# Performance work log

Measured on AMD Instinct MI355X. Metric: run time of the kernel, lower is better.

Reference implementation:

```python
import jax, jax.numpy as jnp
import numpy as np

N_QUBITS = 8

def _ry(theta):
    # PennyLane RY = exp(-i theta Y/2) = [[c,-s],[s,c]]
    c = jnp.cos(theta / 2).astype(jnp.complex64)
    s = jnp.sin(theta / 2).astype(jnp.complex64)
    return jnp.stack([jnp.stack([c, -s], -1), jnp.stack([s, c], -1)], -2)

def _rz(theta):
    # PennyLane RZ = diag(e^{-i theta/2}, e^{i theta/2})
    ph = jnp.exp(-0.5j * theta.astype(jnp.complex64))
    z = jnp.zeros_like(ph)
    return jnp.stack([jnp.stack([ph, z], -1), jnp.stack([z, jnp.conj(ph)], -1)], -2)

def _apply_1q(state, U, wire):
    # state: (B, 2,...,2); U: (2,2) or (B,2,2)
    state = jnp.moveaxis(state, wire + 1, -1)
    if U.ndim == 3:
        state = jnp.einsum('bij,b...j->b...i', U, state)
    else:
        state = jnp.einsum('ij,b...j->b...i', U, state)
    return jnp.moveaxis(state, -1, wire + 1)

def _apply_cnot(state, c, t):
    state = jnp.moveaxis(state, (c + 1, t + 1), (-2, -1))
    state = jnp.concatenate([state[..., 0:1, :], state[..., 1:2, ::-1]], axis=-2)
    return jnp.moveaxis(state, (-2, -1), (c + 1, t + 1))

def _circuit(angles, qw):
    # angles: (B, 2*n_qubits), qw: (3, n_qubits, 3)
    B = angles.shape[0]
    state = jnp.zeros((B,) + (2,) * N_QUBITS, jnp.complex64)
    state = state.at[(slice(None),) + (0,) * N_QUBITS].set(1.0)
    for i in range(N_QUBITS):
        state = _apply_1q(state, _ry(angles[:, i]), i)
        state = _apply_1q(state, _rz(angles[:, i + N_QUBITS]), i)
    for layer in range(3):
        for i in range(N_QUBITS):
            phi, theta, omega = qw[layer, i]
            U = _rz(omega) @ _ry(theta) @ _rz(phi)  # Rot(phi,theta,omega)
            state = _apply_1q(state, U, i)
        for i in range(N_QUBITS - 1):
            state = _apply_cnot(state, i, i + 1)
        state = _apply_cnot(state, N_QUBITS - 1, 0)
    probs = jnp.abs(state) ** 2  # (B, 2,...,2) real
    expz = []
    for i in range(N_QUBITS):
        p = probs.sum(axis=tuple(a for a in range(1, N_QUBITS + 1) if a != i + 1))
        expz.append(p[:, 0] - p[:, 1])  # <Z_i> = p(0) - p(1)
    return jnp.stack(expz, -1)


def setup_inputs() -> dict:
    key = jax.random.key(0)
    ks = jax.random.split(key, 10)
    B = 16384
    return {
        'x': jax.random.normal(ks[0], (B, 80), jnp.float32),
        'W1': jax.random.normal(ks[1], (64, 80), jnp.float32) * 0.1,
        'b1': jax.random.normal(ks[2], (64,), jnp.float32) * 0.1,
        'W2': jax.random.normal(ks[3], (32, 64), jnp.float32) * 0.1,
        'b2': jax.random.normal(ks[4], (32,), jnp.float32) * 0.1,
        'W3': jax.random.normal(ks[5], (16, 32), jnp.float32) * 0.1,
        'b3': jax.random.normal(ks[6], (16,), jnp.float32) * 0.1,
        'qw': jax.random.normal(ks[7], (3, 8, 3), jnp.float32),
        'Wp': jax.random.normal(ks[8], (128, 8), jnp.float32) * 0.1,
        'bp': jax.random.normal(ks[9], (128,), jnp.float32) * 0.1,
    }


def reference(x, W1, b1, W2, b2, W3, b3, qw, Wp, bp):
    h = jnp.tanh(x @ W1.T + b1)
    h = jnp.tanh(h @ W2.T + b2)
    angles = h @ W3.T + b3          # (B, 16)
    z = _circuit(angles, qw)        # (B, 8) PauliZ expectations
    return z @ Wp.T + bp            # (B, 128)
```

## Files before the change

kernel.cpp:

```cpp
#include <hip/hip_runtime.h>

typedef float v2f __attribute__((ext_vector_type(2)));

#define WPB 4
#define NE  4

__device__ __forceinline__ float xorf(float v, int sb) {
  return __int_as_float(__float_as_int(v) ^ sb);
}
__device__ __forceinline__ v2f xor2(v2f v, int sb) {
  return (v2f){xorf(v.x, sb), xorf(v.y, sb)};
}

__device__ __forceinline__ void pkfma_ip(v2f a, v2f b, v2f& acc) {
  asm("v_pk_fma_f32 %0, %1, %2, %0" : "+v"(acc) : "v"(a), "v"(b));
}
__device__ __forceinline__ v2f pkmul_bl(v2f c, v2f v) {
  v2f r; asm("v_pk_mul_f32 %0, %1, %2 op_sel:[0,0] op_sel_hi:[0,1]"
             : "=v"(r) : "v"(c), "v"(v)); return r;
}
__device__ __forceinline__ void pkfma_bl(v2f c, v2f v, v2f& acc) {
  asm("v_pk_fma_f32 %0, %1, %2, %0 op_sel:[0,0,0] op_sel_hi:[0,1,1]"
      : "+v"(acc) : "v"(c), "v"(v));
}
__device__ __forceinline__ void pkfma_bl_n(v2f c, v2f v, v2f& acc) {
  asm("v_pk_fma_f32 %0, %1, %2, %0 op_sel:[0,0,0] op_sel_hi:[0,1,1] neg_lo:[1,0,0] neg_hi:[1,0,0]"
      : "+v"(acc) : "v"(c), "v"(v));
}
__device__ __forceinline__ void pkfma_bh_i(v2f c, v2f v, v2f& acc) {
  asm("v_pk_fma_f32 %0, %1, %2, %0 op_sel:[1,1,0] op_sel_hi:[1,0,1] neg_lo:[1,0,0]"
      : "+v"(acc) : "v"(c), "v"(v));
}
__device__ __forceinline__ void pkfma_bh_mi(v2f c, v2f v, v2f& acc) {
  asm("v_pk_fma_f32 %0, %1, %2, %0 op_sel:[1,1,0] op_sel_hi:[1,0,1] neg_hi:[1,0,0]"
      : "+v"(acc) : "v"(c), "v"(v));
}
__device__ __forceinline__ v2f cmul(v2f a, v2f b) {
  v2f r = pkmul_bl(a, b);
  pkfma_bh_i(a, b, r);
  return r;
}

template<int M>
__device__ __forceinline__ float xch(float v, int a32) {
  if constexpr (M == 32)
    return __int_as_float(__builtin_amdgcn_ds_bpermute(a32, __float_as_int(v)));
  else if constexpr (M == 16 || M == 4)
    return __int_as_float(__builtin_amdgcn_ds_swizzle(__float_as_int(v), (M << 10) | 0x1f));
  else if constexpr (M == 8) {
    int i = __float_as_int(v);
    return __int_as_float(__builtin_amdgcn_update_dpp(i, i, 0x128, 0xF, 0xF, false));
  } else if constexpr (M == 2) {
    int i = __float_as_int(v);
    return __int_as_float(__builtin_amdgcn_update_dpp(i, i, 0x4E, 0xF, 0xF, false));
  } else {
    int i = __float_as_int(v);
    return __int_as_float(__builtin_amdgcn_update_dpp(i, i, 0xB1, 0xF, 0xF, false));
  }
}
template<int M>
__device__ __forceinline__ v2f xch2(v2f v, int a32) {
  v2f r; r.x = xch<M>(v.x, a32); r.y = xch<M>(v.y, a32); return r;
}
__device__ __forceinline__ v2f bperm2(int addr, v2f v) {
  v2f r;
  r.x = __int_as_float(__builtin_amdgcn_ds_bpermute(addr, __float_as_int(v.x)));
  r.y = __int_as_float(__builtin_amdgcn_ds_bpermute(addr, __float_as_int(v.y)));
  return r;
}

__device__ __forceinline__ void gpair(v2f& a, v2f& b, v2f P1, v2f P2) {
  v2f na = pkmul_bl(P1, a);
  pkfma_bh_i(P1, a, na);
  pkfma_bl(P2, b, na);
  pkfma_bh_i(P2, b, na);
  v2f nb = pkmul_bl(P1, b);
  pkfma_bh_mi(P1, b, nb);
  pkfma_bl_n(P2, a, nb);
  pkfma_bh_i(P2, a, nb);
  a = na; b = nb;
}
__device__ __forceinline__ v2f glane(v2f a, v2f p, v2f P1, v2f P2) {
  v2f t = pkmul_bl(P1, a);
  pkfma_bh_i(P1, a, t);
  pkfma_bl(P2, p, t);
  pkfma_bh_i(P2, p, t);
  return t;
}

template<int W>
__device__ __forceinline__ void gate_elem(v2f& S0, v2f& S1, v2f& S2, v2f& S3,
                                          v2f P1, v2f P2, int a32) {
  if constexpr (W == 0)      { gpair(S0, S2, P1, P2); gpair(S1, S3, P1, P2); }
  else if constexpr (W == 1) { gpair(S0, S1, P1, P2); gpair(S2, S3, P1, P2); }
  else {
    constexpr int M = 1 << (7 - W);
    v2f p0 = xch2<M>(S0, a32), p1 = xch2<M>(S1, a32),
        p2 = xch2<M>(S2, a32), p3 = xch2<M>(S3, a32);
    S0 = glane(S0, p0, P1, P2); S1 = glane(S1, p1, P1, P2);
    S2 = glane(S2, p2, P1, P2); S3 = glane(S3, p3, P1, P2);
  }
}

__device__ __forceinline__ void build_state(v2f& S0, v2f& S1, v2f& S2, v2f& S3,
                                            const float4* csW, int lane) {
  v2f g2, g3, g4, g5, g6, g7;
  #define BG(q, dst) { float4 c = csW[q]; \
    v2f P1 = (v2f){c.x, c.y}; v2f nc2 = (v2f){-c.z, c.w}; \
    dst = (((lane >> (7 - (q))) & 1) != 0) ? nc2 : P1; }
  BG(2, g2) BG(3, g3) BG(4, g4) BG(5, g5) BG(6, g6) BG(7, g7)
  #undef BG
  v2f common = cmul(cmul(cmul(g2, g3), cmul(g4, g5)), cmul(g6, g7));
  float4 c0 = csW[0], c1 = csW[1];
  v2f P10 = (v2f){c0.x, c0.y}, m0 = (v2f){-c0.z, c0.w};
  v2f P11 = (v2f){c1.x, c1.y}, m1 = (v2f){-c1.z, c1.w};
  S0 = cmul(cmul(P10, P11), common);
  S1 = cmul(cmul(P10, m1 ), common);
  S2 = cmul(cmul(m0 , P11), common);
  S3 = cmul(cmul(m0 , m1 ), common);
}

__device__ __forceinline__ void cnot_ring(v2f& S0, v2f& S1, v2f& S2, v2f& S3,
                                          int addrA, int addrB, int lane) {
  { v2f t = S2; S2 = S3; S3 = t; }
  S0 = bperm2(addrA, S0); S2 = bperm2(addrA, S2);
  S1 = bperm2(addrB, S1); S3 = bperm2(addrB, S3);
  bool c0 = (lane & 1) != 0;
  v2f t0 = S0, t1 = S1;
  S0 = c0 ? S2 : S0; S2 = c0 ? t0 : S2;
  S1 = c0 ? S3 : S1; S3 = c0 ? t1 : S3;
}

__device__ __forceinline__ void readout2(v2f A0, v2f A1, v2f A2, v2f A3,
                                         v2f B0, v2f B1, v2f B2, v2f B3,
                                         int lane, const int* sb, int a32,
                                         v2f& z0, v2f& z1, v2f& z2, v2f& z3,
                                         v2f& z4, v2f& z5, v2f& z6, v2f& z7) {
  v2f p0 = (v2f){fmaf(A0.x,A0.x,A0.y*A0.y), fmaf(B0.x,B0.x,B0.y*B0.y)};
  v2f p1 = (v2f){fmaf(A1.x,A1.x,A1.y*A1.y), fmaf(B1.x,B1.x,B1.y*B1.y)};
  v2f p2 = (v2f){fmaf(A2.x,A2.x,A2.y*A2.y), fmaf(B2.x,B2.x,B2.y*B2.y)};
  v2f p3 = (v2f){fmaf(A3.x,A3.x,A3.y*A3.y), fmaf(B3.x,B3.x,B3.y*B3.y)};
  v2f E = (p0 + p3) - (p1 + p2);
  v2f F = (p0 + p2) - (p1 + p3);
  v2f Fv = xor2(F, (__popc(lane) & 1) << 31);
  v2f Sm = E, d1, d2, d3, d4, d5, d6;
  { v2f p = xch2<32>(Sm, a32); d1 = xor2(Sm - p, sb[0]); Sm += p; }
  { v2f p = xch2<16>(Sm, a32); Sm += p;
    v2f q = xch2<16>(d1, a32); d2 = xor2(d1 - q, sb[1]); d1 += q; }
  { v2f p = xch2<8>(Sm, a32); Sm += p;
    v2f q = xch2<8>(d1, a32); d1 += q;
    v2f r = xch2<8>(d2, a32); d3 = xor2(d2 - r, sb[2]); d2 += r; }
  { v2f p = xch2<4>(Sm, a32); Sm += p;
    v2f q = xch2<4>(d1, a32); d1 += q;
    v2f r = xch2<4>(d2, a32); d2 += r;
    v2f t = xch2<4>(d3, a32); d4 = xor2(d3 - t, sb[3]); d3 += t; }
  { v2f p = xch2<2>(Sm, a32); Sm += p;
    v2f q = xch2<2>(d1, a32); d1 += q;
    v2f r = xch2<2>(d2, a32); d2 += r;
    v2f t = xch2<2>(d3, a32); d3 += t;
    v2f w = xch2<2>(d4, a32); d5 = xor2(d4 - w, sb[4]); d4 += w; }
  { v2f p = xch2<1>(Sm, a32); Sm += p;
    v2f q = xch2<1>(d1, a32); d1 += q;
    v2f r = xch2<1>(d2, a32); d2 += r;
    v2f t = xch2<1>(d3, a32); d3 += t;
    v2f w = xch2<1>(d4, a32); d4 += w;
    v2f v = xch2<1>(d5, a32); d6 = xor2(d5 - v, sb[5]); d5 += v; }
  Fv += xch2<32>(Fv, a32); Fv += xch2<16>(Fv, a32); Fv += xch2<8>(Fv, a32);
  Fv += xch2<4>(Fv, a32);  Fv += xch2<2>(Fv, a32);  Fv += xch2<1>(Fv, a32);
  z0 = Fv; z1 = Sm; z2 = d1; z3 = d2;
  z4 = d3; z5 = d4; z6 = d5; z7 = d6;
}

__device__ __forceinline__ float fast_tanh(float x) {
  float e = __expf(2.f * x);
  return 1.f - 2.f * __builtin_amdgcn_rcpf(e + 1.f);
}
__device__ __forceinline__ v2f vlo(float4 v) { return (v2f){v.x, v.y}; }
__device__ __forceinline__ v2f vhi(float4 v) { return (v2f){v.z, v.w}; }

__global__ void prep_rot_kernel(const float* __restrict__ qw, float* __restrict__ U) {
  int t = threadIdx.x;
  if (t < 24) {
    float phi = qw[t*3+0], theta = qw[t*3+1], omega = qw[t*3+2];
    float st, ct; sincosf(0.5f*theta, &st, &ct);
    float sa, ca; sincosf(0.5f*(phi+omega), &sa, &ca);
    float sd, cd; sincosf(0.5f*(phi-omega), &sd, &cd);
    float4 o; o.x = ct*ca; o.y = -ct*sa; o.z = -st*cd; o.w = -st*sd;
    ((float4*)U)[t] = o;
  }
}

__global__ __launch_bounds__(64*WPB, 4) void qblock_kernel(
    const float* __restrict__ x,  const float* __restrict__ W1, const float* __restrict__ b1,
    const float* __restrict__ W2, const float* __restrict__ b2,
    const float* __restrict__ W3, const float* __restrict__ b3,
    const float* __restrict__ Urot, const float* __restrict__ Wp, const float* __restrict__ bp,
    float* __restrict__ out, int B4)
{
  __shared__ float  h1s[WPB][NE][64];
  __shared__ float  h2s[WPB][NE][32];
  __shared__ v2f    cs [WPB][NE][16];
  __shared__ float4 csW[WPB][NE][8];

  const int lane = threadIdx.x & 63;
  const int wv   = threadIdx.x >> 6;
  int bw = blockIdx.x * WPB + wv;
  if (bw >= B4) bw = B4 - 1;
  bw = __builtin_amdgcn_readfirstlane(bw);
  const int e0 = NE * bw;
  const v2f* Ug2 = (const v2f*)Urot;

  {
    const float4* wr = (const float4*)(W1 + lane * 80);
    float bv = b1[lane];
    v2f a0A = (v2f){bv,0.f}, a1A = (v2f){0.f,0.f};
    v2f a0B = a0A, a1B = a1A, a0C = a0A, a1C = a1A, a0D = a0A, a1D = a1A;
    #pragma unroll
    for (int k = 0; k < 20; ++k) {
      float4 wk = wr[k];
      #define L1E(E, e) { \
        float4 xk = ((const float4*)(x + (size_t)(e0 + (e)) * 80))[k]; \
        pkfma_ip(vlo(xk), vlo(wk), a0##E); pkfma_ip(vhi(xk), vhi(wk), a1##E); }
      L1E(A,0) L1E(B,1) L1E(C,2) L1E(D,3)
      #undef L1E
    }
    h1s[wv][0][lane] = fast_tanh((a0A.x + a0A.y) + (a1A.x + a1A.y));
    h1s[wv][1][lane] = fast_tanh((a0B.x + a0B.y) + (a1B.x + a1B.y));
    h1s[wv][2][lane] = fast_tanh((a0C.x + a0C.y) + (a1C.x + a1C.y));
    h1s[wv][3][lane] = fast_tanh((a0D.x + a0D.y) + (a1D.x + a1D.y));
  }
  __threadfence_block();

  {
    const int ep = lane >> 5, row = lane & 31;
    const float4* wr = (const float4*)(W2 + row * 64);
    const float4* hvA = (const float4*)(&h1s[wv][2*ep+0][0]);
    const float4* hvB = (const float4*)(&h1s[wv][2*ep+1][0]);
    v2f aA0 = (v2f){b2[row], 0.f}, aA1 = (v2f){0.f, 0.f};
    v2f aB0 = aA0, aB1 = aA1;
    #pragma unroll
    for (int k = 0; k < 16; ++k) {
      float4 wk = wr[k], hA = hvA[k], hB = hvB[k];
      pkfma_ip(vlo(hA), vlo(wk), aA0); pkfma_ip(vhi(hA), vhi(wk), aA1);
      pkfma_ip(vlo(hB), vlo(wk), aB0); pkfma_ip(vhi(hB), vhi(wk), aB1);
    }
    h2s[wv][2*ep+0][row] = fast_tanh((aA0.x + aA0.y) + (aA1.x + aA1.y));
    h2s[wv][2*ep+1][row] = fast_tanh((aB0.x + aB0.y) + (aB1.x + aB1.y));
  }
  __threadfence_block();

  {
    const int e = lane >> 4, row = lane & 15;
    const float4* hv = (const float4*)(&h2s[wv][e][0]);
    const float4* wr = (const float4*)(W3 + row * 32);
    v2f ac0 = (v2f){b3[row], 0.f}, ac1 = (v2f){0.f, 0.f};
    #pragma unroll
    for (int k = 0; k < 8; ++k) {
      float4 hk = hv[k], wk = wr[k];
      pkfma_ip(vlo(hk), vlo(wk), ac0);
      pkfma_ip(vhi(hk), vhi(wk), ac1);
    }
    float sh, ch; __sincosf(0.5f * ((ac0.x + ac0.y) + (ac1.x + ac1.y)), &sh, &ch);
    cs[wv][e][row] = (v2f){ch, sh};
  }
  __threadfence_block();

  if (lane < 32) {
    const int e = lane >> 3, k = lane & 7;
    v2f yy = cs[wv][e][k], zz = cs[wv][e][k + 8];
    v2f u1 = (v2f){  yy.x * zz.x, -yy.x * zz.y };
    v2f u2 = (v2f){ -yy.y * zz.x,  yy.y * zz.y };
    v2f cu1 = (v2f){ u1.x, -u1.y };
    v2f cu2 = (v2f){ u2.x, -u2.y };
    v2f r1 = Ug2[2 * k], r2 = Ug2[2 * k + 1];
    v2f P1c = cmul(r1, u1);
    pkfma_bl_n(r2, cu2, P1c);
    pkfma_bh_mi(r2, cu2, P1c);
    v2f P2c = cmul(r1, u2);
    pkfma_bl(r2, cu1, P2c);
    pkfma_bh_i(r2, cu1, P2c);
    csW[wv][e][k] = make_float4(P1c.x, P1c.y, P2c.x, P2c.y);
  }
  __threadfence_block();

  const int a32 = (lane ^ 32) << 2;
  const int sb[6] = { (lane&32)<<26, (lane&16)<<27, (lane&8)<<28,
                      (lane&4)<<29, (lane&2)<<30, (lane&1)<<31 };
  const int addrA = ((lane ^ (lane >> 1)) & 63) << 2;
  const int addrB = addrA ^ 128;

  v2f sA0, sA1, sA2, sA3, sB0, sB1, sB2, sB3;
  v2f sC0, sC1, sC2, sC3, sD0, sD1, sD2, sD3;
  build_state(sA0, sA1, sA2, sA3, &csW[wv][0][0], lane);
  build_state(sB0, sB1, sB2, sB3, &csW[wv][1][0], lane);
  build_state(sC0, sC1, sC2, sC3, &csW[wv][2][0], lane);
  build_state(sD0, sD1, sD2, sD3, &csW[wv][3][0], lane);
  #define RING_ALL \
    cnot_ring(sA0, sA1, sA2, sA3, addrA, addrB, lane); \
    cnot_ring(sB0, sB1, sB2, sB3, addrA, addrB, lane); \
    cnot_ring(sC0, sC1, sC2, sC3, addrA, addrB, lane); \
    cnot_ring(sD0, sD1, sD2, sD3, addrA, addrB, lane);
  RING_ALL

  #define LG(l, i) { \
    v2f P1 = Ug2[((l)*8+(i))*2], P2 = Ug2[((l)*8+(i))*2+1]; \
    if constexpr ((i) >= 2) { \
      P1.y = xorf(P1.y, sb[(i)-2]); P2.x = xorf(P2.x, sb[(i)-2]); } \
    gate_elem<i>(sA0, sA1, sA2, sA3, P1, P2, a32); \
    gate_elem<i>(sB0, sB1, sB2, sB3, P1, P2, a32); \
    gate_elem<i>(sC0, sC1, sC2, sC3, P1, P2, a32); \
    gate_elem<i>(sD0, sD1, sD2, sD3, P1, P2, a32); }
  LG(1,0) LG(1,1) LG(1,2) LG(1,3) LG(1,4) LG(1,5) LG(1,6) LG(1,7)
  RING_ALL
  LG(2,0) LG(2,1) LG(2,2) LG(2,3) LG(2,4) LG(2,5) LG(2,6) LG(2,7)
  #undef LG
  #undef RING_ALL

  const int r0 = 2 * lane;
  const float4* wp = (const float4*)(Wp + r0 * 8);
  float4 w0v = wp[0], w1v = wp[1], w2v = wp[2], w3v = wp[3];
  float2 bpv = ((const float2*)bp)[lane];
  #define PROJ_STORE(eA, eB) { \
    v2f o0 = (v2f){bpv.x, bpv.x}; \
    v2f o1 = (v2f){bpv.y, bpv.y}; \
    o0 += z0*w0v.x + z1*w0v.y + z2*w0v.z + z3*w0v.w \
        + z4*w1v.x + z5*w1v.y + z6*w1v.z + z7*w1v.w; \
    o1 += z0*w2v.x + z1*w2v.y + z2*w2v.z + z3*w2v.w \
        + z4*w3v.x + z5*w3v.y + z6*w3v.z + z7*w3v.w; \
    ((float2*)(out + (size_t)(e0 + (eA)) * 128))[lane] = make_float2(o0.x, o1.x); \
    ((float2*)(out + (size_t)(e0 + (eB)) * 128))[lane] = make_float2(o0.y, o1.y); }
  {
    v2f z0, z1, z2, z3, z4, z5, z6, z7;
    readout2(sA0, sA1, sA2, sA3, sB0, sB1, sB2, sB3, lane, sb, a32,
             z0, z1, z2, z3, z4, z5, z6, z7);
    PROJ_STORE(0, 1)
  }
  {
    v2f z0, z1, z2, z3, z4, z5, z6, z7;
    readout2(sC0, sC1, sC2, sC3, sD0, sD1, sD2, sD3, lane, sb, a32,
             z0, z1, z2, z3, z4, z5, z6, z7);
    PROJ_STORE(2, 3)
  }
  #undef PROJ_STORE
}

extern "C" void kernel_launch(void* const* d_in, const int* in_sizes, int n_in,
                              void* d_out, int out_size, void* d_ws, size_t ws_size,
                              hipStream_t stream) {
  const float* x  = (const float*)d_in[0];
  const float* W1 = (const float*)d_in[1];
  const float* b1 = (const float*)d_in[2];
  const float* W2 = (const float*)d_in[3];
  const float* b2 = (const float*)d_in[4];
  const float* W3 = (const float*)d_in[5];
  const float* b3 = (const float*)d_in[6];
  const float* qw = (const float*)d_in[7];
  const float* Wp = (const float*)d_in[8];
  const float* bp = (const float*)d_in[9];
  float* out = (float*)d_out;
  float* Urot = (float*)d_ws;

  const int B = in_sizes[0] / 80;
  const int B4 = B / NE;
  prep_rot_kernel<<<1, 64, 0, stream>>>(qw, Urot);
  const int grid = (B4 + WPB - 1) / WPB;
  qblock_kernel<<<grid, 64 * WPB, 0, stream>>>(x, W1, b1, W2, b2, W3, b3,
                                               Urot, Wp, bp, out, B4);
}
```

Before: 41.79 us.

## Split fused kernel into MLP prep kernel and per-element circuit kernel

Splits the single fused kernel in two. The first kernel computes the MLP and the initial rotation coefficients and writes them to a global workspace. The second runs the quantum circuit with one element per wavefront instead of four, which reduces register pressure and gives four times as many waves for latency hiding. The cost is an extra launch, a global round trip for the coefficients, and the loss of the four-element interleaving that gave instruction-level parallelism and packed readout.

```diff
diff --git a/kernel.cpp b/kernel.cpp
--- a/kernel.cpp
+++ b/kernel.cpp
@@ -7,9 +7,6 @@
 
 __device__ __forceinline__ float xorf(float v, int sb) {
   return __int_as_float(__float_as_int(v) ^ sb);
-}
-__device__ __forceinline__ v2f xor2(v2f v, int sb) {
-  return (v2f){xorf(v.x, sb), xorf(v.y, sb)};
 }
 
 __device__ __forceinline__ void pkfma_ip(v2f a, v2f b, v2f& acc) {
@@ -131,46 +128,6 @@
   S1 = c0 ? S3 : S1; S3 = c0 ? t1 : S3;
 }
 
-__device__ __forceinline__ void readout2(v2f A0, v2f A1, v2f A2, v2f A3,
-                                         v2f B0, v2f B1, v2f B2, v2f B3,
-                                         int lane, const int* sb, int a32,
-                                         v2f& z0, v2f& z1, v2f& z2, v2f& z3,
-                                         v2f& z4, v2f& z5, v2f& z6, v2f& z7) {
-  v2f p0 = (v2f){fmaf(A0.x,A0.x,A0.y*A0.y), fmaf(B0.x,B0.x,B0.y*B0.y)};
-  v2f p1 = (v2f){fmaf(A1.x,A1.x,A1.y*A1.y), fmaf(B1.x,B1.x,B1.y*B1.y)};
-  v2f p2 = (v2f){fmaf(A2.x,A2.x,A2.y*A2.y), fmaf(B2.x,B2.x,B2.y*B2.y)};
-  v2f p3 = (v2f){fmaf(A3.x,A3.x,A3.y*A3.y), fmaf(B3.x,B3.x,B3.y*B3.y)};
-  v2f E = (p0 + p3) - (p1 + p2);
-  v2f F = (p0 + p2) - (p1 + p3);
-  v2f Fv = xor2(F, (__popc(lane) & 1) << 31);
-  v2f Sm = E, d1, d2, d3, d4, d5, d6;
-  { v2f p = xch2<32>(Sm, a32); d1 = xor2(Sm - p, sb[0]); Sm += p; }
-  { v2f p = xch2<16>(Sm, a32); Sm += p;
-    v2f q = xch2<16>(d1, a32); d2 = xor2(d1 - q, sb[1]); d1 += q; }
-  { v2f p = xch2<8>(Sm, a32); Sm += p;
-    v2f q = xch2<8>(d1, a32); d1 += q;
-    v2f r = xch2<8>(d2, a32); d3 = xor2(d2 - r, sb[2]); d2 += r; }
-  { v2f p = xch2<4>(Sm, a32); Sm += p;
-    v2f q = xch2<4>(d1, a32); d1 += q;
-    v2f r = xch2<4>(d2, a32); d2 += r;
-    v2f t = xch2<4>(d3, a32); d4 = xor2(d3 - t, sb[3]); d3 += t; }
-  { v2f p = xch2<2>(Sm, a32); Sm += p;
-    v2f q = xch2<2>(d1, a32); d1 += q;
-    v2f r = xch2<2>(d2, a32); d2 += r;
-    v2f t = xch2<2>(d3, a32); d3 += t;
-    v2f w = xch2<2>(d4, a32); d5 = xor2(d4 - w, sb[4]); d4 += w; }
-  { v2f p = xch2<1>(Sm, a32); Sm += p;
-    v2f q = xch2<1>(d1, a32); d1 += q;
-    v2f r = xch2<1>(d2, a32); d2 += r;
-    v2f t = xch2<1>(d3, a32); d3 += t;
-    v2f w = xch2<1>(d4, a32); d4 += w;
-    v2f v = xch2<1>(d5, a32); d6 = xor2(d5 - v, sb[5]); d5 += v; }
-  Fv += xch2<32>(Fv, a32); Fv += xch2<16>(Fv, a32); Fv += xch2<8>(Fv, a32);
-  Fv += xch2<4>(Fv, a32);  Fv += xch2<2>(Fv, a32);  Fv += xch2<1>(Fv, a32);
-  z0 = Fv; z1 = Sm; z2 = d1; z3 = d2;
-  z4 = d3; z5 = d4; z6 = d5; z7 = d6;
-}
-
 __device__ __forceinline__ float fast_tanh(float x) {
   float e = __expf(2.f * x);
   return 1.f - 2.f * __builtin_amdgcn_rcpf(e + 1.f);
@@ -190,17 +147,15 @@
   }
 }
 
-__global__ __launch_bounds__(64*WPB, 4) void qblock_kernel(
+__global__ __launch_bounds__(64*WPB) void prep_kernel(
     const float* __restrict__ x,  const float* __restrict__ W1, const float* __restrict__ b1,
     const float* __restrict__ W2, const float* __restrict__ b2,
     const float* __restrict__ W3, const float* __restrict__ b3,
-    const float* __restrict__ Urot, const float* __restrict__ Wp, const float* __restrict__ bp,
-    float* __restrict__ out, int B4)
+    const float* __restrict__ Urot, float4* __restrict__ csWg, int B4)
 {
-  __shared__ float  h1s[WPB][NE][64];
-  __shared__ float  h2s[WPB][NE][32];
-  __shared__ v2f    cs [WPB][NE][16];
-  __shared__ float4 csW[WPB][NE][8];
+  __shared__ float h1s[WPB][NE][64];
+  __shared__ float h2s[WPB][NE][32];
+  __shared__ v2f   cs [WPB][NE][16];
 
   const int lane = threadIdx.x & 63;
   const int wv   = threadIdx.x >> 6;
@@ -279,9 +234,21 @@
     v2f P2c = cmul(r1, u2);
     pkfma_bl(r2, cu1, P2c);
     pkfma_bh_i(r2, cu1, P2c);
-    csW[wv][e][k] = make_float4(P1c.x, P1c.y, P2c.x, P2c.y);
-  }
-  __threadfence_block();
+    csWg[(size_t)(e0 + e) * 8 + k] = make_float4(P1c.x, P1c.y, P2c.x, P2c.y);
+  }
+}
+
+__global__ __launch_bounds__(64*WPB) void qcirc_kernel(
+    const float* __restrict__ Urot, const float4* __restrict__ csWg,
+    const float* __restrict__ Wp, const float* __restrict__ bp,
+    float* __restrict__ out, int B)
+{
+  const int lane = threadIdx.x & 63;
+  const int wv   = threadIdx.x >> 6;
+  int e = blockIdx.x * WPB + wv;
+  if (e >= B) e = B - 1;
+  e = __builtin_amdgcn_readfirstlane(e);
+  const v2f* Ug2 = (const v2f*)Urot;
 
   const int a32 = (lane ^ 32) << 2;
   const int sb[6] = { (lane&32)<<26, (lane&16)<<27, (lane&8)<<28,
@@ -289,59 +256,62 @@
   const int addrA = ((lane ^ (lane >> 1)) & 63) << 2;
   const int addrB = addrA ^ 128;
 
-  v2f sA0, sA1, sA2, sA3, sB0, sB1, sB2, sB3;
-  v2f sC0, sC1, sC2, sC3, sD0, sD1, sD2, sD3;
-  build_state(sA0, sA1, sA2, sA3, &csW[wv][0][0], lane);
-  build_state(sB0, sB1, sB2, sB3, &csW[wv][1][0], lane);
-  build_state(sC0, sC1, sC2, sC3, &csW[wv][2][0], lane);
-  build_state(sD0, sD1, sD2, sD3, &csW[wv][3][0], lane);
-  #define RING_ALL \
-    cnot_ring(sA0, sA1, sA2, sA3, addrA, addrB, lane); \
-    cnot_ring(sB0, sB1, sB2, sB3, addrA, addrB, lane); \
-    cnot_ring(sC0, sC1, sC2, sC3, addrA, addrB, lane); \
-    cnot_ring(sD0, sD1, sD2, sD3, addrA, addrB, lane);
-  RING_ALL
+  v2f s0, s1, s2, s3;
+  build_state(s0, s1, s2, s3, csWg + (size_t)e * 8, lane);
+  cnot_ring(s0, s1, s2, s3, addrA, addrB, lane);
 
   #define LG(l, i) { \
     v2f P1 = Ug2[((l)*8+(i))*2], P2 = Ug2[((l)*8+(i))*2+1]; \
     if constexpr ((i) >= 2) { \
       P1.y = xorf(P1.y, sb[(i)-2]); P2.x = xorf(P2.x, sb[(i)-2]); } \
-    gate_elem<i>(sA0, sA1, sA2, sA3, P1, P2, a32); \
-    gate_elem<i>(sB0, sB1, sB2, sB3, P1, P2, a32); \
-    gate_elem<i>(sC0, sC1, sC2, sC3, P1, P2, a32); \
-    gate_elem<i>(sD0, sD1, sD2, sD3, P1, P2, a32); }
+    gate_elem<i>(s0, s1, s2, s3, P1, P2, a32); }
   LG(1,0) LG(1,1) LG(1,2) LG(1,3) LG(1,4) LG(1,5) LG(1,6) LG(1,7)
-  RING_ALL
+  cnot_ring(s0, s1, s2, s3, addrA, addrB, lane);
   LG(2,0) LG(2,1) LG(2,2) LG(2,3) LG(2,4) LG(2,5) LG(2,6) LG(2,7)
   #undef LG
-  #undef RING_ALL
+
+  float p0 = s0.x*s0.x + s0.y*s0.y;
+  float p1 = s1.x*s1.x + s1.y*s1.y;
+  float p2 = s2.x*s2.x + s2.y*s2.y;
+  float p3 = s3.x*s3.x + s3.y*s3.y;
+  float E = (p0 + p3) - (p1 + p2);
+  float F = (p0 + p2) - (p1 + p3);
+  float Fv = xorf(F, (__popc(lane) & 1) << 31);
+  float Sm = E, d1, d2, d3, d4, d5, d6;
+  { float p = xch<32>(Sm, a32); d1 = xorf(Sm - p, sb[0]); Sm += p; }
+  { float p = xch<16>(Sm, a32); Sm += p;
+    float q = xch<16>(d1, a32); d2 = xorf(d1 - q, sb[1]); d1 += q; }
+  { float p = xch<8>(Sm, a32); Sm += p;
+    float q = xch<8>(d1, a32); d1 += q;
+    float r = xch<8>(d2, a32); d3 = xorf(d2 - r, sb[2]); d2 += r; }
+  { float p = xch<4>(Sm, a32); Sm += p;
+    float q = xch<4>(d1, a32); d1 += q;
+    float r = xch<4>(d2, a32); d2 += r;
+    float t = xch<4>(d3, a32); d4 = xorf(d3 - t, sb[3]); d3 += t; }
+  { float p = xch<2>(Sm, a32); Sm += p;
+    float q = xch<2>(d1, a32); d1 += q;
+    float r = xch<2>(d2, a32); d2 += r;
+    float t = xch<2>(d3, a32); d3 += t;
+    float w = xch<2>(d4, a32); d5 = xorf(d4 - w, sb[4]); d4 += w; }
+  { float p = xch<1>(Sm, a32); Sm += p;
+    float q = xch<1>(d1, a32); d1 += q;
+    float r = xch<1>(d2, a32); d2 += r;
+    float t = xch<1>(d3, a32); d3 += t;
+    float w = xch<1>(d4, a32); d4 += w;
+    float v = xch<1>(d5, a32); d6 = xorf(d5 - v, sb[5]); d5 += v; }
+  Fv += xch<32>(Fv, a32); Fv += xch<16>(Fv, a32); Fv += xch<8>(Fv, a32);
+  Fv += xch<4>(Fv, a32);  Fv += xch<2>(Fv, a32);  Fv += xch<1>(Fv, a32);
+  const float z0 = Fv, z1 = Sm, z2 = d1, z3 = d2, z4 = d3, z5 = d4, z6 = d5, z7 = d6;
 
   const int r0 = 2 * lane;
   const float4* wp = (const float4*)(Wp + r0 * 8);
   float4 w0v = wp[0], w1v = wp[1], w2v = wp[2], w3v = wp[3];
   float2 bpv = ((const float2*)bp)[lane];
-  #define PROJ_STORE(eA, eB) { \
-    v2f o0 = (v2f){bpv.x, bpv.x}; \
-    v2f o1 = (v2f){bpv.y, bpv.y}; \
-    o0 += z0*w0v.x + z1*w0v.y + z2*w0v.z + z3*w0v.w \
-        + z4*w1v.x + z5*w1v.y + z6*w1v.z + z7*w1v.w; \
-    o1 += z0*w2v.x + z1*w2v.y + z2*w2v.z + z3*w2v.w \
-        + z4*w3v.x + z5*w3v.y + z6*w3v.z + z7*w3v.w; \
-    ((float2*)(out + (size_t)(e0 + (eA)) * 128))[lane] = make_float2(o0.x, o1.x); \
-    ((float2*)(out + (size_t)(e0 + (eB)) * 128))[lane] = make_float2(o0.y, o1.y); }
-  {
-    v2f z0, z1, z2, z3, z4, z5, z6, z7;
-    readout2(sA0, sA1, sA2, sA3, sB0, sB1, sB2, sB3, lane, sb, a32,
-             z0, z1, z2, z3, z4, z5, z6, z7);
-    PROJ_STORE(0, 1)
-  }
-  {
-    v2f z0, z1, z2, z3, z4, z5, z6, z7;
-    readout2(sC0, sC1, sC2, sC3, sD0, sD1, sD2, sD3, lane, sb, a32,
-             z0, z1, z2, z3, z4, z5, z6, z7);
-    PROJ_STORE(2, 3)
-  }
-  #undef PROJ_STORE
+  float o0 = bpv.x + z0*w0v.x + z1*w0v.y + z2*w0v.z + z3*w0v.w
+                   + z4*w1v.x + z5*w1v.y + z6*w1v.z + z7*w1v.w;
+  float o1 = bpv.y + z0*w2v.x + z1*w2v.y + z2*w2v.z + z3*w2v.w
+                   + z4*w3v.x + z5*w3v.y + z6*w3v.z + z7*w3v.w;
+  ((float2*)(out + (size_t)e * 128))[lane] = make_float2(o0, o1);
 }
 
 extern "C" void kernel_launch(void* const* d_in, const int* in_sizes, int n_in,
@@ -359,11 +329,13 @@
   const float* bp = (const float*)d_in[9];
   float* out = (float*)d_out;
   float* Urot = (float*)d_ws;
+  float4* csWg = (float4*)((char*)d_ws + 1024);
 
   const int B = in_sizes[0] / 80;
   const int B4 = B / NE;
   prep_rot_kernel<<<1, 64, 0, stream>>>(qw, Urot);
-  const int grid = (B4 + WPB - 1) / WPB;
-  qblock_kernel<<<grid, 64 * WPB, 0, stream>>>(x, W1, b1, W2, b2, W3, b3,
-                                               Urot, Wp, bp, out, B4);
-}
+  prep_kernel<<<(B4 + WPB - 1) / WPB, 64 * WPB, 0, stream>>>(
+      x, W1, b1, W2, b2, W3, b3, Urot, csWg, B4);
+  qcirc_kernel<<<(B + WPB - 1) / WPB, 64 * WPB, 0, stream>>>(
+      Urot, csWg, Wp, bp, out, B);
+}
```

After: 46.87 us. +12.2%, slower.

## Replace per-sample gate simulation with bf16 MFMA complex matmul against precomputed circuit unitary

Applied to the files above, without the earlier changes.

The fixed trainable part of the circuit (two variational layers plus CNOT rings) is now precomputed once per call as a 256x256 complex unitary in bf16 by a separate kernel. Each block builds the encoded product states of 16 samples in LDS and multiplies them by the unitary using bf16 MFMA, then reduces signed probabilities into Z expectations. W1/W2 are also transposed into LDS for coalesced MLP loads. This trades the shuffle-heavy per-gate work for matrix-core throughput, at the cost of bf16 precision loss, an extra kernel launch and heavy global/LDS traffic streaming the 256 KB unitary through every block.

```diff
diff --git a/kernel.cpp b/kernel.cpp
--- a/kernel.cpp
+++ b/kernel.cpp
@@ -1,15 +1,16 @@
 #include <hip/hip_runtime.h>
 
 typedef float v2f __attribute__((ext_vector_type(2)));
+typedef float f32x4 __attribute__((ext_vector_type(4)));
+typedef short bf16x8 __attribute__((ext_vector_type(8)));
 
 #define WPB 4
 #define NE  4
 
+#define SE(E,N) s##E##N
+
 __device__ __forceinline__ float xorf(float v, int sb) {
   return __int_as_float(__float_as_int(v) ^ sb);
-}
-__device__ __forceinline__ v2f xor2(v2f v, int sb) {
-  return (v2f){xorf(v.x, sb), xorf(v.y, sb)};
 }
 
 __device__ __forceinline__ void pkfma_ip(v2f a, v2f b, v2f& acc) {
@@ -87,7 +88,6 @@
   pkfma_bh_i(P2, p, t);
   return t;
 }
-
 template<int W>
 __device__ __forceinline__ void gate_elem(v2f& S0, v2f& S1, v2f& S2, v2f& S3,
                                           v2f P1, v2f P2, int a32) {
@@ -101,7 +101,15 @@
     S2 = glane(S2, p2, P1, P2); S3 = glane(S3, p3, P1, P2);
   }
 }
-
+__device__ __forceinline__ void cnot_ring(v2f& S0, v2f& S1, v2f& S2, v2f& S3,
+                                          int addrA, int addrB, int lane) {
+  { v2f t = S2; S2 = S3; S3 = t; }
+  v2f q0 = bperm2(addrA, S0), q2 = bperm2(addrA, S2);
+  v2f q1 = bperm2(addrB, S1), q3 = bperm2(addrB, S3);
+  bool c0 = (lane & 1) != 0;
+  S0 = c0 ? q2 : q0; S2 = c0 ? q0 : q2;
+  S1 = c0 ? q3 : q1; S3 = c0 ? q1 : q3;
+}
 __device__ __forceinline__ void build_state(v2f& S0, v2f& S1, v2f& S2, v2f& S3,
                                             const float4* csW, int lane) {
   v2f g2, g3, g4, g5, g6, g7;
@@ -120,63 +128,17 @@
   S3 = cmul(cmul(m0 , m1 ), common);
 }
 
-__device__ __forceinline__ void cnot_ring(v2f& S0, v2f& S1, v2f& S2, v2f& S3,
-                                          int addrA, int addrB, int lane) {
-  { v2f t = S2; S2 = S3; S3 = t; }
-  S0 = bperm2(addrA, S0); S2 = bperm2(addrA, S2);
-  S1 = bperm2(addrB, S1); S3 = bperm2(addrB, S3);
-  bool c0 = (lane & 1) != 0;
-  v2f t0 = S0, t1 = S1;
-  S0 = c0 ? S2 : S0; S2 = c0 ? t0 : S2;
-  S1 = c0 ? S3 : S1; S3 = c0 ? t1 : S3;
-}
-
-__device__ __forceinline__ void readout2(v2f A0, v2f A1, v2f A2, v2f A3,
-                                         v2f B0, v2f B1, v2f B2, v2f B3,
-                                         int lane, const int* sb, int a32,
-                                         v2f& z0, v2f& z1, v2f& z2, v2f& z3,
-                                         v2f& z4, v2f& z5, v2f& z6, v2f& z7) {
-  v2f p0 = (v2f){fmaf(A0.x,A0.x,A0.y*A0.y), fmaf(B0.x,B0.x,B0.y*B0.y)};
-  v2f p1 = (v2f){fmaf(A1.x,A1.x,A1.y*A1.y), fmaf(B1.x,B1.x,B1.y*B1.y)};
-  v2f p2 = (v2f){fmaf(A2.x,A2.x,A2.y*A2.y), fmaf(B2.x,B2.x,B2.y*B2.y)};
-  v2f p3 = (v2f){fmaf(A3.x,A3.x,A3.y*A3.y), fmaf(B3.x,B3.x,B3.y*B3.y)};
-  v2f E = (p0 + p3) - (p1 + p2);
-  v2f F = (p0 + p2) - (p1 + p3);
-  v2f Fv = xor2(F, (__popc(lane) & 1) << 31);
-  v2f Sm = E, d1, d2, d3, d4, d5, d6;
-  { v2f p = xch2<32>(Sm, a32); d1 = xor2(Sm - p, sb[0]); Sm += p; }
-  { v2f p = xch2<16>(Sm, a32); Sm += p;
-    v2f q = xch2<16>(d1, a32); d2 = xor2(d1 - q, sb[1]); d1 += q; }
-  { v2f p = xch2<8>(Sm, a32); Sm += p;
-    v2f q = xch2<8>(d1, a32); d1 += q;
-    v2f r = xch2<8>(d2, a32); d3 = xor2(d2 - r, sb[2]); d2 += r; }
-  { v2f p = xch2<4>(Sm, a32); Sm += p;
-    v2f q = xch2<4>(d1, a32); d1 += q;
-    v2f r = xch2<4>(d2, a32); d2 += r;
-    v2f t = xch2<4>(d3, a32); d4 = xor2(d3 - t, sb[3]); d3 += t; }
-  { v2f p = xch2<2>(Sm, a32); Sm += p;
-    v2f q = xch2<2>(d1, a32); d1 += q;
-    v2f r = xch2<2>(d2, a32); d2 += r;
-    v2f t = xch2<2>(d3, a32); d3 += t;
-    v2f w = xch2<2>(d4, a32); d5 = xor2(d4 - w, sb[4]); d4 += w; }
-  { v2f p = xch2<1>(Sm, a32); Sm += p;
-    v2f q = xch2<1>(d1, a32); d1 += q;
-    v2f r = xch2<1>(d2, a32); d2 += r;
-    v2f t = xch2<1>(d3, a32); d3 += t;
-    v2f w = xch2<1>(d4, a32); d4 += w;
-    v2f v = xch2<1>(d5, a32); d6 = xor2(d5 - v, sb[5]); d5 += v; }
-  Fv += xch2<32>(Fv, a32); Fv += xch2<16>(Fv, a32); Fv += xch2<8>(Fv, a32);
-  Fv += xch2<4>(Fv, a32);  Fv += xch2<2>(Fv, a32);  Fv += xch2<1>(Fv, a32);
-  z0 = Fv; z1 = Sm; z2 = d1; z3 = d2;
-  z4 = d3; z5 = d4; z6 = d5; z7 = d6;
-}
-
 __device__ __forceinline__ float fast_tanh(float x) {
   float e = __expf(2.f * x);
   return 1.f - 2.f * __builtin_amdgcn_rcpf(e + 1.f);
 }
 __device__ __forceinline__ v2f vlo(float4 v) { return (v2f){v.x, v.y}; }
 __device__ __forceinline__ v2f vhi(float4 v) { return (v2f){v.z, v.w}; }
+__device__ __forceinline__ unsigned short bf16rne(float f) {
+  unsigned int u = __float_as_uint(f);
+  u += 0x7fffu + ((u >> 16) & 1u);
+  return (unsigned short)(u >> 16);
+}
 
 __global__ void prep_rot_kernel(const float* __restrict__ qw, float* __restrict__ U) {
   int t = threadIdx.x;
@@ -190,68 +152,161 @@
   }
 }
 
-__global__ __launch_bounds__(64*WPB, 4) void qblock_kernel(
+__global__ __launch_bounds__(256) void prep_U_kernel(
+    const float* __restrict__ Urot,
+    unsigned short* __restrict__ UTre, unsigned short* __restrict__ UTim)
+{
+  const int lane = threadIdx.x & 63;
+  const int wv   = threadIdx.x >> 6;
+  const int base = blockIdx.x * 16 + wv * 4;
+  const v2f* Ug2 = (const v2f*)Urot;
+
+  const int a32 = (lane ^ 32) << 2;
+  const int sb[6] = { (lane&32)<<26, (lane&16)<<27, (lane&8)<<28,
+                      (lane&4)<<29, (lane&2)<<30, (lane&1)<<31 };
+  const int addrA = ((lane ^ (lane >> 1)) & 63) << 2;
+  const int addrB = addrA ^ 128;
+
+  v2f sA0,sA1,sA2,sA3, sB0,sB1,sB2,sB3, sC0,sC1,sC2,sC3, sD0,sD1,sD2,sD3;
+  #define INITB(E, q) { int b = base + (q); \
+    float one = (lane == (b & 63)) ? 1.f : 0.f; \
+    SE(E,0) = (v2f){((b>>6)==0)?one:0.f, 0.f}; \
+    SE(E,1) = (v2f){((b>>6)==1)?one:0.f, 0.f}; \
+    SE(E,2) = (v2f){((b>>6)==2)?one:0.f, 0.f}; \
+    SE(E,3) = (v2f){((b>>6)==3)?one:0.f, 0.f}; }
+  INITB(A,0) INITB(B,1) INITB(C,2) INITB(D,3)
+  #undef INITB
+
+  #define RING_ALL \
+    cnot_ring(sA0, sA1, sA2, sA3, addrA, addrB, lane); \
+    cnot_ring(sB0, sB1, sB2, sB3, addrA, addrB, lane); \
+    cnot_ring(sC0, sC1, sC2, sC3, addrA, addrB, lane); \
+    cnot_ring(sD0, sD1, sD2, sD3, addrA, addrB, lane);
+  #define LG(l, i) { \
+    v2f P1 = Ug2[((l)*8+(i))*2], P2 = Ug2[((l)*8+(i))*2+1]; \
+    if constexpr ((i) >= 2) { \
+      P1.y = xorf(P1.y, sb[(i)-2]); P2.x = xorf(P2.x, sb[(i)-2]); } \
+    gate_elem<i>(sA0, sA1, sA2, sA3, P1, P2, a32); \
+    gate_elem<i>(sB0, sB1, sB2, sB3, P1, P2, a32); \
+    gate_elem<i>(sC0, sC1, sC2, sC3, P1, P2, a32); \
+    gate_elem<i>(sD0, sD1, sD2, sD3, P1, P2, a32); }
+  RING_ALL
+  LG(1,0) LG(1,1) LG(1,2) LG(1,3) LG(1,4) LG(1,5) LG(1,6) LG(1,7)
+  RING_ALL
+  LG(2,0) LG(2,1) LG(2,2) LG(2,3) LG(2,4) LG(2,5) LG(2,6) LG(2,7)
+  #undef LG
+  #undef RING_ALL
+
+  #define STOREB(E, q) { int b = base + (q); \
+    UTre[(0*64+lane)*256 + b] = bf16rne(SE(E,0).x); UTim[(0*64+lane)*256 + b] = bf16rne(SE(E,0).y); \
+    UTre[(1*64+lane)*256 + b] = bf16rne(SE(E,1).x); UTim[(1*64+lane)*256 + b] = bf16rne(SE(E,1).y); \
+    UTre[(2*64+lane)*256 + b] = bf16rne(SE(E,2).x); UTim[(2*64+lane)*256 + b] = bf16rne(SE(E,2).y); \
+    UTre[(3*64+lane)*256 + b] = bf16rne(SE(E,3).x); UTim[(3*64+lane)*256 + b] = bf16rne(SE(E,3).y); }
+  STOREB(A,0) STOREB(B,1) STOREB(C,2) STOREB(D,3)
+  #undef STOREB
+}
+
+#define OFF_ARE 0
+#define OFF_AIM 8192
+#define OFF_BRE 16384
+#define OFF_BIM 32768
+#define OFF_W1T 0
+#define OFF_W2T 20480
+#define OFF_H1  28672
+#define OFF_H2  32768
+#define OFF_CS  34816
+#define OFF_CSW 36864
+#define OFF_ZL  0
+
+__global__ __launch_bounds__(256) void qblock_kernel(
     const float* __restrict__ x,  const float* __restrict__ W1, const float* __restrict__ b1,
     const float* __restrict__ W2, const float* __restrict__ b2,
     const float* __restrict__ W3, const float* __restrict__ b3,
-    const float* __restrict__ Urot, const float* __restrict__ Wp, const float* __restrict__ bp,
-    float* __restrict__ out, int B4)
+    const float* __restrict__ Urot,
+    const unsigned short* __restrict__ UTre, const unsigned short* __restrict__ UTim,
+    const float* __restrict__ Wp, const float* __restrict__ bp,
+    float* __restrict__ out)
 {
-  __shared__ float  h1s[WPB][NE][64];
-  __shared__ float  h2s[WPB][NE][32];
-  __shared__ v2f    cs [WPB][NE][16];
-  __shared__ float4 csW[WPB][NE][8];
-
-  const int lane = threadIdx.x & 63;
-  const int wv   = threadIdx.x >> 6;
-  int bw = blockIdx.x * WPB + wv;
-  if (bw >= B4) bw = B4 - 1;
-  bw = __builtin_amdgcn_readfirstlane(bw);
-  const int e0 = NE * bw;
+  __shared__ char smem[49152];
+  v2f*            W1t = (v2f*)(smem + OFF_W1T);
+  v2f*            W2t = (v2f*)(smem + OFF_W2T);
+  float*          h1s = (float*)(smem + OFF_H1);
+  float*          h2s = (float*)(smem + OFF_H2);
+  v2f*            csv = (v2f*)(smem + OFF_CS);
+  float4*         csW = (float4*)(smem + OFF_CSW);
+  unsigned short* Are = (unsigned short*)(smem + OFF_ARE);
+  unsigned short* Aim = (unsigned short*)(smem + OFF_AIM);
+  unsigned short* Bre = (unsigned short*)(smem + OFF_BRE);
+  unsigned short* Bim = (unsigned short*)(smem + OFF_BIM);
+  float*          zl  = (float*)(smem + OFF_ZL);
+
+  const int tid  = threadIdx.x;
+  const int lane = tid & 63;
+  const int wv   = tid >> 6;
+  const int e0   = blockIdx.x * 16;
+  const int ew   = e0 + wv * NE;
   const v2f* Ug2 = (const v2f*)Urot;
 
   {
-    const float4* wr = (const float4*)(W1 + lane * 80);
+    const v2f* W1f2 = (const v2f*)W1;
+    #pragma unroll
+    for (int i = 0; i < 10; ++i) {
+      int j = i * 256 + tid;
+      int r = j / 40, kk = j - r * 40;
+      W1t[kk * 64 + r] = W1f2[j];
+    }
+    const v2f* W2f2 = (const v2f*)W2;
+    #pragma unroll
+    for (int i = 0; i < 4; ++i) {
+      int j = i * 256 + tid;
+      int r = j >> 5, kk = j & 31;
+      W2t[kk * 32 + r] = W2f2[j];
+    }
+  }
+  __syncthreads();
+
+  {
+    const v2f* xA = (const v2f*)(x + (size_t)(ew + 0) * 80);
+    const v2f* xB = (const v2f*)(x + (size_t)(ew + 1) * 80);
+    const v2f* xC = (const v2f*)(x + (size_t)(ew + 2) * 80);
+    const v2f* xD = (const v2f*)(x + (size_t)(ew + 3) * 80);
     float bv = b1[lane];
-    v2f a0A = (v2f){bv,0.f}, a1A = (v2f){0.f,0.f};
-    v2f a0B = a0A, a1B = a1A, a0C = a0A, a1C = a1A, a0D = a0A, a1D = a1A;
-    #pragma unroll
-    for (int k = 0; k < 20; ++k) {
-      float4 wk = wr[k];
-      #define L1E(E, e) { \
-        float4 xk = ((const float4*)(x + (size_t)(e0 + (e)) * 80))[k]; \
-        pkfma_ip(vlo(xk), vlo(wk), a0##E); pkfma_ip(vhi(xk), vhi(wk), a1##E); }
-      L1E(A,0) L1E(B,1) L1E(C,2) L1E(D,3)
-      #undef L1E
-    }
-    h1s[wv][0][lane] = fast_tanh((a0A.x + a0A.y) + (a1A.x + a1A.y));
-    h1s[wv][1][lane] = fast_tanh((a0B.x + a0B.y) + (a1B.x + a1B.y));
-    h1s[wv][2][lane] = fast_tanh((a0C.x + a0C.y) + (a1C.x + a1C.y));
-    h1s[wv][3][lane] = fast_tanh((a0D.x + a0D.y) + (a1D.x + a1D.y));
+    v2f aA = (v2f){bv, 0.f}, aB = aA, aC = aA, aD = aA;
+    #pragma unroll 8
+    for (int kk = 0; kk < 40; ++kk) {
+      v2f w = W1t[kk * 64 + lane];
+      pkfma_ip(w, xA[kk], aA);
+      pkfma_ip(w, xB[kk], aB);
+      pkfma_ip(w, xC[kk], aC);
+      pkfma_ip(w, xD[kk], aD);
+    }
+    h1s[(wv*4+0)*64 + lane] = fast_tanh(aA.x + aA.y);
+    h1s[(wv*4+1)*64 + lane] = fast_tanh(aB.x + aB.y);
+    h1s[(wv*4+2)*64 + lane] = fast_tanh(aC.x + aC.y);
+    h1s[(wv*4+3)*64 + lane] = fast_tanh(aD.x + aD.y);
   }
   __threadfence_block();
 
   {
     const int ep = lane >> 5, row = lane & 31;
-    const float4* wr = (const float4*)(W2 + row * 64);
-    const float4* hvA = (const float4*)(&h1s[wv][2*ep+0][0]);
-    const float4* hvB = (const float4*)(&h1s[wv][2*ep+1][0]);
-    v2f aA0 = (v2f){b2[row], 0.f}, aA1 = (v2f){0.f, 0.f};
-    v2f aB0 = aA0, aB1 = aA1;
-    #pragma unroll
-    for (int k = 0; k < 16; ++k) {
-      float4 wk = wr[k], hA = hvA[k], hB = hvB[k];
-      pkfma_ip(vlo(hA), vlo(wk), aA0); pkfma_ip(vhi(hA), vhi(wk), aA1);
-      pkfma_ip(vlo(hB), vlo(wk), aB0); pkfma_ip(vhi(hB), vhi(wk), aB1);
-    }
-    h2s[wv][2*ep+0][row] = fast_tanh((aA0.x + aA0.y) + (aA1.x + aA1.y));
-    h2s[wv][2*ep+1][row] = fast_tanh((aB0.x + aB0.y) + (aB1.x + aB1.y));
+    const v2f* hA = (const v2f*)(&h1s[(wv*4 + 2*ep+0)*64]);
+    const v2f* hB = (const v2f*)(&h1s[(wv*4 + 2*ep+1)*64]);
+    float bv = b2[row];
+    v2f aA = (v2f){bv, 0.f}, aB = aA;
+    #pragma unroll 8
+    for (int kk = 0; kk < 32; ++kk) {
+      v2f w = W2t[kk * 32 + row];
+      pkfma_ip(w, hA[kk], aA);
+      pkfma_ip(w, hB[kk], aB);
+    }
+    h2s[(wv*4 + 2*ep+0)*32 + row] = fast_tanh(aA.x + aA.y);
+    h2s[(wv*4 + 2*ep+1)*32 + row] = fast_tanh(aB.x + aB.y);
   }
   __threadfence_block();
 
   {
     const int e = lane >> 4, row = lane & 15;
-    const float4* hv = (const float4*)(&h2s[wv][e][0]);
+    const float4* hv = (const float4*)(&h2s[(wv*4 + e)*32]);
     const float4* wr = (const float4*)(W3 + row * 32);
     v2f ac0 = (v2f){b3[row], 0.f}, ac1 = (v2f){0.f, 0.f};
     #pragma unroll
@@ -261,13 +316,13 @@
       pkfma_ip(vhi(hk), vhi(wk), ac1);
     }
     float sh, ch; __sincosf(0.5f * ((ac0.x + ac0.y) + (ac1.x + ac1.y)), &sh, &ch);
-    cs[wv][e][row] = (v2f){ch, sh};
+    csv[(wv*4 + e)*16 + row] = (v2f){ch, sh};
   }
   __threadfence_block();
 
   if (lane < 32) {
     const int e = lane >> 3, k = lane & 7;
-    v2f yy = cs[wv][e][k], zz = cs[wv][e][k + 8];
+    v2f yy = csv[(wv*4 + e)*16 + k], zz = csv[(wv*4 + e)*16 + k + 8];
     v2f u1 = (v2f){  yy.x * zz.x, -yy.x * zz.y };
     v2f u2 = (v2f){ -yy.y * zz.x,  yy.y * zz.y };
     v2f cu1 = (v2f){ u1.x, -u1.y };
@@ -279,69 +334,110 @@
     v2f P2c = cmul(r1, u2);
     pkfma_bl(r2, cu1, P2c);
     pkfma_bh_i(r2, cu1, P2c);
-    csW[wv][e][k] = make_float4(P1c.x, P1c.y, P2c.x, P2c.y);
+    csW[(wv*4 + e)*8 + k] = make_float4(P1c.x, P1c.y, P2c.x, P2c.y);
   }
   __threadfence_block();
-
+  __syncthreads();
+
+  #pragma unroll
+  for (int q = 0; q < NE; ++q) {
+    v2f S0, S1, S2, S3;
+    build_state(S0, S1, S2, S3, (const float4*)&csW[(wv*4 + q)*8], lane);
+    const int row = wv*4 + q, swz = (row & 7) << 3;
+    #define AW(r, S) { int n = (r)*64 + lane; int idx = ((row)*256 + n) ^ swz; \
+      Are[idx] = bf16rne(S.x); Aim[idx] = bf16rne(S.y); }
+    AW(0, S0) AW(1, S1) AW(2, S2) AW(3, S3)
+    #undef AW
+  }
+
+  f32x4 cre0 = {0,0,0,0}, cre1 = cre0, cre2 = cre0, cre3 = cre0;
+  f32x4 cim0 = cre0, cim1 = cre0, cim2 = cre0, cim3 = cre0;
+  for (int ks = 0; ks < 8; ++ks) {
+    __syncthreads();
+    #pragma unroll
+    for (int r = 0; r < 8; ++r) {
+      int n = r * 32 + (tid >> 3);
+      int kk8 = (tid & 7) * 4;
+      uint2 dre = *(const uint2*)(UTre + n * 256 + ks * 32 + kk8);
+      uint2 dim = *(const uint2*)(UTim + n * 256 + ks * 32 + kk8);
+      int bidx = (n * 32 + kk8) ^ ((n & 7) << 3);
+      *(uint2*)(Bre + bidx) = dre;
+      *(uint2*)(Bim + bidx) = dim;
+    }
+    __syncthreads();
+    const int arow = lane & 15;
+    const int aidx = (arow * 256 + ks * 32 + (lane >> 4) * 8) ^ ((arow & 7) << 3);
+    bf16x8 are = *(const bf16x8*)(Are + aidx);
+    bf16x8 aim = *(const bf16x8*)(Aim + aidx);
+    bf16x8 aimn = aim ^ (short)0x8000;
+    #define NT(t, CRE, CIM) { \
+      int n = wv * 64 + (t) * 16 + (lane & 15); \
+      int bidx2 = (n * 32 + (lane >> 4) * 8) ^ ((n & 7) << 3); \
+      bf16x8 bre = *(const bf16x8*)(Bre + bidx2); \
+      bf16x8 bim = *(const bf16x8*)(Bim + bidx2); \
+      CRE = __builtin_amdgcn_mfma_f32_16x16x32_bf16(are,  bre, CRE, 0, 0, 0); \
+      CRE = __builtin_amdgcn_mfma_f32_16x16x32_bf16(aimn, bim, CRE, 0, 0, 0); \
+      CIM = __builtin_amdgcn_mfma_f32_16x16x32_bf16(are,  bim, CIM, 0, 0, 0); \
+      CIM = __builtin_amdgcn_mfma_f32_16x16x32_bf16(aim,  bre, CIM, 0, 0, 0); }
+    NT(0, cre0, cim0) NT(1, cre1, cim1) NT(2, cre2, cim2) NT(3, cre3, cim3)
+    #undef NT
+  }
+
+  float zacc[32];
+  #pragma unroll
+  for (int i = 0; i < 32; ++i) zacc[i] = 0.f;
   const int a32 = (lane ^ 32) << 2;
-  const int sb[6] = { (lane&32)<<26, (lane&16)<<27, (lane&8)<<28,
-                      (lane&4)<<29, (lane&2)<<30, (lane&1)<<31 };
-  const int addrA = ((lane ^ (lane >> 1)) & 63) << 2;
-  const int addrB = addrA ^ 128;
-
-  v2f sA0, sA1, sA2, sA3, sB0, sB1, sB2, sB3;
-  v2f sC0, sC1, sC2, sC3, sD0, sD1, sD2, sD3;
-  build_state(sA0, sA1, sA2, sA3, &csW[wv][0][0], lane);
-  build_state(sB0, sB1, sB2, sB3, &csW[wv][1][0], lane);
-  build_state(sC0, sC1, sC2, sC3, &csW[wv][2][0], lane);
-  build_state(sD0, sD1, sD2, sD3, &csW[wv][3][0], lane);
-  #define RING_ALL \
-    cnot_ring(sA0, sA1, sA2, sA3, addrA, addrB, lane); \
-    cnot_ring(sB0, sB1, sB2, sB3, addrA, addrB, lane); \
-    cnot_ring(sC0, sC1, sC2, sC3, addrA, addrB, lane); \
-    cnot_ring(sD0, sD1, sD2, sD3, addrA, addrB, lane);
-  RING_ALL
-
-  #define LG(l, i) { \
-    v2f P1 = Ug2[((l)*8+(i))*2], P2 = Ug2[((l)*8+(i))*2+1]; \
-    if constexpr ((i) >= 2) { \
-      P1.y = xorf(P1.y, sb[(i)-2]); P2.x = xorf(P2.x, sb[(i)-2]); } \
-    gate_elem<i>(sA0, sA1, sA2, sA3, P1, P2, a32); \
-    gate_elem<i>(sB0, sB1, sB2, sB3, P1, P2, a32); \
-    gate_elem<i>(sC0, sC1, sC2, sC3, P1, P2, a32); \
-    gate_elem<i>(sD0, sD1, sD2, sD3, P1, P2, a32); }
-  LG(1,0) LG(1,1) LG(1,2) LG(1,3) LG(1,4) LG(1,5) LG(1,6) LG(1,7)
-  RING_ALL
-  LG(2,0) LG(2,1) LG(2,2) LG(2,3) LG(2,4) LG(2,5) LG(2,6) LG(2,7)
-  #undef LG
-  #undef RING_ALL
+  #define ZT(t, CRE, CIM) { \
+    int nn = wv * 64 + (t) * 16 + (lane & 15); \
+    int sg[8]; \
+    sg[0] = (__popc(nn & 127) & 1) << 31; \
+    _Pragma("unroll") \
+    for (int j = 1; j < 8; ++j) sg[j] = (__popc(nn >> (7 - j)) & 1) << 31; \
+    _Pragma("unroll") \
+    for (int r = 0; r < 4; ++r) { \
+      float p = CRE[r] * CRE[r] + CIM[r] * CIM[r]; \
+      _Pragma("unroll") \
+      for (int j = 0; j < 8; ++j) zacc[r * 8 + j] += xorf(p, sg[j]); } }
+  ZT(0, cre0, cim0) ZT(1, cre1, cim1) ZT(2, cre2, cim2) ZT(3, cre3, cim3)
+  #undef ZT
+  #pragma unroll
+  for (int i = 0; i < 32; ++i) zacc[i] += xch<8>(zacc[i], a32);
+  #pragma unroll
+  for (int i = 0; i < 32; ++i) zacc[i] += xch<4>(zacc[i], a32);
+  #pragma unroll
+  for (int i = 0; i < 32; ++i) zacc[i] += xch<2>(zacc[i], a32);
+  #pragma unroll
+  for (int i = 0; i < 32; ++i) zacc[i] += xch<1>(zacc[i], a32);
+
+  __syncthreads();
+  if ((lane & 15) == 0) {
+    const int eb = (lane >> 4) * 4;
+    #pragma unroll
+    for (int r = 0; r < 4; ++r)
+      #pragma unroll
+      for (int j = 0; j < 8; ++j)
+        zl[(wv * 16 + eb + r) * 8 + j] = zacc[r * 8 + j];
+  }
+  __syncthreads();
 
   const int r0 = 2 * lane;
   const float4* wp = (const float4*)(Wp + r0 * 8);
   float4 w0v = wp[0], w1v = wp[1], w2v = wp[2], w3v = wp[3];
   float2 bpv = ((const float2*)bp)[lane];
-  #define PROJ_STORE(eA, eB) { \
-    v2f o0 = (v2f){bpv.x, bpv.x}; \
-    v2f o1 = (v2f){bpv.y, bpv.y}; \
-    o0 += z0*w0v.x + z1*w0v.y + z2*w0v.z + z3*w0v.w \
-        + z4*w1v.x + z5*w1v.y + z6*w1v.z + z7*w1v.w; \
-    o1 += z0*w2v.x + z1*w2v.y + z2*w2v.z + z3*w2v.w \
-        + z4*w3v.x + z5*w3v.y + z6*w3v.z + z7*w3v.w; \
-    ((float2*)(out + (size_t)(e0 + (eA)) * 128))[lane] = make_float2(o0.x, o1.x); \
-    ((float2*)(out + (size_t)(e0 + (eB)) * 128))[lane] = make_float2(o0.y, o1.y); }
-  {
-    v2f z0, z1, z2, z3, z4, z5, z6, z7;
-    readout2(sA0, sA1, sA2, sA3, sB0, sB1, sB2, sB3, lane, sb, a32,
-             z0, z1, z2, z3, z4, z5, z6, z7);
-    PROJ_STORE(0, 1)
-  }
-  {
-    v2f z0, z1, z2, z3, z4, z5, z6, z7;
-    readout2(sC0, sC1, sC2, sC3, sD0, sD1, sD2, sD3, lane, sb, a32,
-             z0, z1, z2, z3, z4, z5, z6, z7);
-    PROJ_STORE(2, 3)
-  }
-  #undef PROJ_STORE
+  #pragma unroll
+  for (int q = 0; q < NE; ++q) {
+    const int e = wv * 4 + q;
+    float z[8];
+    #pragma unroll
+    for (int j = 0; j < 8; ++j)
+      z[j] = zl[(0*16 + e)*8 + j] + zl[(1*16 + e)*8 + j]
+           + zl[(2*16 + e)*8 + j] + zl[(3*16 + e)*8 + j];
+    float o0 = bpv.x + z[0]*w0v.x + z[1]*w0v.y + z[2]*w0v.z + z[3]*w0v.w
+                     + z[4]*w1v.x + z[5]*w1v.y + z[6]*w1v.z + z[7]*w1v.w;
+    float o1 = bpv.y + z[0]*w2v.x + z[1]*w2v.y + z[2]*w2v.z + z[3]*w2v.w
+                     + z[4]*w3v.x + z[5]*w3v.y + z[6]*w3v.z + z[7]*w3v.w;
+    ((float2*)(out + (size_t)(e0 + e) * 128))[lane] = make_float2(o0, o1);
+  }
 }
 
 extern "C" void kernel_launch(void* const* d_in, const int* in_sizes, int n_in,
@@ -359,11 +455,12 @@
   const float* bp = (const float*)d_in[9];
   float* out = (float*)d_out;
   float* Urot = (float*)d_ws;
+  unsigned short* UTre = (unsigned short*)((char*)d_ws + 4096);
+  unsigned short* UTim = (unsigned short*)((char*)d_ws + 4096 + 131072);
 
   const int B = in_sizes[0] / 80;
-  const int B4 = B / NE;
   prep_rot_kernel<<<1, 64, 0, stream>>>(qw, Urot);
-  const int grid = (B4 + WPB - 1) / WPB;
-  qblock_kernel<<<grid, 64 * WPB, 0, stream>>>(x, W1, b1, W2, b2, W3, b3,
-                                               Urot, Wp, bp, out, B4);
-}
+  prep_U_kernel<<<16, 256, 0, stream>>>(Urot, UTre, UTim);
+  qblock_kernel<<<B / 16, 256, 0, stream>>>(x, W1, b1, W2, b2, W3, b3,
+                                            Urot, UTre, UTim, Wp, bp, out);
+}
```

Result: slower. 64.84 us (+55.1%).
